# Kernel optimization log

Hardware: AMD Instinct MI355X
Metric: run time of the kernel (lower is better)

Reference implementation:

```python
import jax, jax.numpy as jnp
import numpy as np
from jax import lax

B, S = 256, 512
CHAR_NUM, CLASS_NUM, OUTPUT_NUM, WORD_EMBED, H = 10, 10, 64, 32, 128
EPS = 1e-12


def setup_inputs() -> dict:
    key = jax.random.key(0)
    ks = jax.random.split(key, 16)
    def nrm(k, shape, s=0.05):
        return jax.random.normal(k, shape, dtype=jnp.float32) * s
    return {
        "char_ids": jax.random.randint(ks[0], (B, S), 0, CHAR_NUM),
        "word_ids": jax.random.randint(ks[1], (B, S), 0, CHAR_NUM),
        "subject_ids": jax.random.randint(ks[2], (B, 2), 0, S),
        "emb_char": nrm(ks[3], (CHAR_NUM, OUTPUT_NUM)),
        "emb_word": nrm(ks[4], (CHAR_NUM, WORD_EMBED)),
        "Wwc": nrm(ks[5], (WORD_EMBED, OUTPUT_NUM)),
        "bwc": jnp.zeros((OUTPUT_NUM,), jnp.float32),
        "l1_Wx": nrm(ks[6], (OUTPUT_NUM, 4 * H)),
        "l1_Wh": nrm(ks[7], (H, 4 * H)),
        "l1_b": jnp.zeros((4 * H,), jnp.float32),
        "l2_Wx": nrm(ks[8], (H, 4 * H)),
        "l2_Wh": nrm(ks[9], (H, 4 * H)),
        "l2_b": jnp.zeros((4 * H,), jnp.float32),
        "beta_W": nrm(ks[10], (2 * H, H)),
        "beta_b": jnp.zeros((H,), jnp.float32),
        "gamma_W": nrm(ks[11], (2 * H, H)),
        "gamma_b": jnp.zeros((H,), jnp.float32),
        "sub_W": nrm(ks[12], (H, 2)),
        "sub_b": jnp.zeros((2,), jnp.float32),
        "po_W": nrm(ks[13], (H, 2 * CLASS_NUM)),
        "po_b": jnp.zeros((2 * CLASS_NUM,), jnp.float32),
    }


def _lstm_cell(x, h, c, Wx, Wh, b):
    # Keras LSTMCell: gates ordered i, f, g(cell), o
    z = x @ Wx + h @ Wh + b
    i, f, g, o = jnp.split(z, 4, axis=-1)
    c_new = jax.nn.sigmoid(f) * c + jax.nn.sigmoid(i) * jnp.tanh(g)
    h_new = jax.nn.sigmoid(o) * jnp.tanh(c_new)
    return h_new, c_new


def reference(char_ids, word_ids, subject_ids,
              emb_char, emb_word, Wwc, bwc,
              l1_Wx, l1_Wh, l1_b, l2_Wx, l2_Wh, l2_b,
              beta_W, beta_b, gamma_W, gamma_b,
              sub_W, sub_b, po_W, po_b):
    b, s = char_ids.shape
    # NOTE: source passes mask = (char_ids == 0) to the RNN; in Keras, mask True
    # means the step IS processed, so only positions with id==0 update state.
    step_mask = (char_ids == 0)  # [B, S] bool

    emb = emb_char[char_ids] + (emb_word[word_ids] @ Wwc + bwc)  # [B, S, 64]

    def step(carry, inp):
        h1, c1, h2, c2 = carry
        xt, mt = inp  # xt [B, 64], mt [B]
        h1n, c1n = _lstm_cell(xt, h1, c1, l1_Wx, l1_Wh, l1_b)
        h2n, c2n = _lstm_cell(h1n, h2, c2, l2_Wx, l2_Wh, l2_b)
        m = mt[:, None]
        h1 = jnp.where(m, h1n, h1)
        c1 = jnp.where(m, c1n, c1)
        h2 = jnp.where(m, h2n, h2)
        c2 = jnp.where(m, c2n, c2)
        return (h1, c1, h2, c2), h2

    z = jnp.zeros((b, H), emb.dtype)
    _, outs = lax.scan(step, (z, z, z, z),
                       (emb.transpose(1, 0, 2), step_mask.T))
    sent = outs.transpose(1, 0, 2)  # [B, S, 128]

    # vectorized batch_gather (replaces eager numpy per-row loop)
    bidx = jnp.arange(b)
    sub_start = sent[bidx, subject_ids[:, 0]]  # [B, 128]
    sub_end = sent[bidx, subject_ids[:, 1]]    # [B, 128]
    subject = jnp.concatenate([sub_start, sub_end], axis=1)  # [B, 256]

    # conditional layer norm
    beta = subject @ beta_W + beta_b    # [B, 128]
    gamma = subject @ gamma_W + gamma_b
    u = jnp.mean(sent, axis=-1, keepdims=True)
    v = jnp.mean((sent - u) ** 2, axis=-1, keepdims=True)
    xhat = (sent - u) / jnp.sqrt(v + EPS)
    context = gamma[:, None, :] * xhat + beta[:, None, :]  # [B, S, 128]

    # (transformer_encoder LSTM(32) output is dead code in the source; omitted)
    sub_preds = sent @ sub_W + sub_b                     # [B, S, 2]
    po_preds = (context @ po_W + po_b).reshape(b, -1, CLASS_NUM, 2)  # [B, S, 10, 2]
    return sub_preds, po_preds
```

## Files before the change

kernel.cpp:

```cpp
#include <hip/hip_runtime.h>
#include <cstdint>
#include <cstddef>


#define SLOTS 192

typedef _Float16 f16x2 __attribute__((ext_vector_type(2)));

__device__ __forceinline__ f16x2 as_h2(unsigned int v) {
    union { unsigned int u; f16x2 h; } x; x.u = v; return x.h;
}

#if __has_builtin(__builtin_amdgcn_fdot2)
__device__ __forceinline__ float fdot2(f16x2 a, f16x2 b, float c) {
    return __builtin_amdgcn_fdot2(a, b, c, false);
}
#else
__device__ __forceinline__ float fdot2(f16x2 a, f16x2 b, float c) {
    return c + (float)a.x * (float)b.x + (float)a.y * (float)b.y;
}
#endif

__device__ __forceinline__ float fast_rcp(float x) {
#if __has_builtin(__builtin_amdgcn_rcpf)
    return __builtin_amdgcn_rcpf(x);
#else
    return 1.f / x;
#endif
}
__device__ __forceinline__ float sigm(float x) {
    x = fminf(fmaxf(x, -30.f), 30.f);
    return fast_rcp(1.f + __expf(-x));
}
__device__ __forceinline__ float tanh_fast(float x) {
    x = fminf(fmaxf(x, -15.f), 15.f);
    float e = __expf(-2.f * x);
    return (1.f - e) * fast_rcp(1.f + e);
}

__device__ __forceinline__ float dpp_bfly4(float v) {
    union { float f; int i; } a, b;
    a.f = v;
    b.i = __builtin_amdgcn_update_dpp(0, a.i, 0xB1, 0xf, 0xf, true);
    a.f += b.f;
    b.i = __builtin_amdgcn_update_dpp(0, a.i, 0x4E, 0xf, 0xf, true);
    a.f += b.f;
    return a.f;
}

__device__ __forceinline__ float dot_u4(float s, const uint4 h, const uint4 w) {
    s = fdot2(as_h2(h.x), as_h2(w.x), s);
    s = fdot2(as_h2(h.y), as_h2(w.y), s);
    s = fdot2(as_h2(h.z), as_h2(w.z), s);
    s = fdot2(as_h2(h.w), as_h2(w.w), s);
    return s;
}

__global__ void k_xw1(const float* __restrict__ emb_char,
                      const float* __restrict__ emb_word,
                      const float* __restrict__ Wwc,
                      const float* __restrict__ bwc,
                      const float* __restrict__ l1_Wx,
                      const float* __restrict__ l1_b,
                      float* __restrict__ XW1) {
    __shared__ float xw[64];
    const int w = blockIdx.x;
    const int T = threadIdx.x;
    if (T < 64) {
        float acc = emb_char[T] + bwc[T];
        for (int m = 0; m < 32; ++m) acc += emb_word[w * 32 + m] * Wwc[m * 64 + T];
        xw[T] = acc;
    }
    __syncthreads();
    float acc = l1_b[T];
    for (int k = 0; k < 64; ++k) acc += xw[k] * l1_Wx[k * 512 + T];
    XW1[w * 512 + T] = acc;
}

__global__ void k_pack2(const float* __restrict__ l1_Wh,
                        const float* __restrict__ l2_Wx,
                        const float* __restrict__ l2_Wh,
                        uint4* __restrict__ W1H, uint4* __restrict__ W2H) {
    const int gid = blockIdx.x * blockDim.x + threadIdx.x;
    union { uint4 qv; f16x2 h[4]; } out;
    if (gid < 8192) {
        const int t = gid >> 4, i = gid & 15;
        const int q = t & 3, u = t >> 2;
        const int j = i >> 2, m = i & 3;
        const int col = u + 128 * j;
        for (int e = 0; e < 4; ++e) {
            const int k = 32 * q + 2 * (4 * m + e);
            f16x2 p;
            p.x = (_Float16)l1_Wh[k * 512 + col];
            p.y = (_Float16)l1_Wh[(k + 1) * 512 + col];
            out.h[e] = p;
        }
        W1H[gid] = out.qv;
    } else {
        const int gid2 = gid - 8192;
        const int t = gid2 >> 5, i = gid2 & 31;
        const int q = t & 3, u = t >> 2;
        const int ph = i >> 4, jm = i & 15;
        const int j = jm >> 2, m = jm & 3;
        const int col = u + 128 * j;
        const float* __restrict__ src = ph ? l2_Wx : l2_Wh;
        for (int e = 0; e < 4; ++e) {
            const int k = 32 * q + 2 * (4 * m + e);
            f16x2 p;
            p.x = (_Float16)src[k * 512 + col];
            p.y = (_Float16)src[(k + 1) * 512 + col];
            out.h[e] = p;
        }
        W2H[gid2] = out.qv;
    }
}

__global__ __launch_bounds__(512, 2) void k_lstm(
    const int* __restrict__ char_ids, const int* __restrict__ word_ids,
    const float* __restrict__ XW1, const uint4* __restrict__ W1H,
    const uint4* __restrict__ W2H, const float* __restrict__ l2_b,
    float* __restrict__ hbuf, unsigned short* __restrict__ idxbuf)
{
    const int b    = blockIdx.x;
    const int T    = threadIdx.x;
    const int lane = T & 63;
    const int wv   = T >> 6;
    const int q    = T & 3;
    const int u    = T >> 2;

    __shared__ int   charL[512];
    __shared__ int   wordL[512];
    __shared__ float XW1L[5120];
    __shared__ __align__(16) _Float16 h1f[2][128];
    __shared__ __align__(16) _Float16 h2f[128];
    __shared__ short actT[512];
    __shared__ int   ccnt[8];

    charL[T] = char_ids[b * 512 + T];
    wordL[T] = word_ids[b * 512 + T];
#pragma unroll
    for (int i = 0; i < 10; ++i) XW1L[i * 512 + T] = XW1[i * 512 + T];
    __syncthreads();

    const bool act = (charL[T] == 0);
    const unsigned long long bmask = __ballot(act);
    if (lane == 0) ccnt[wv] = (int)__popcll(bmask);
    __syncthreads();
    int base = 0;
    for (int i = 0; i < wv; ++i) base += ccnt[i];
    int tot = base;
    for (int i = wv; i < 8; ++i) tot += ccnt[i];
    if (act) actT[base + (int)__popcll(bmask & ((1ull << lane) - 1ull))] = (short)T;
    {
        int cin = base + (int)__popcll(bmask & ((2ull << lane) - 1ull));
        idxbuf[b * 512 + T] = (unsigned short)(cin < SLOTS - 1 ? cin : SLOTS - 1);
    }
    const int nact = tot;

    if (T < 128) {
        h1f[0][T] = (_Float16)0.f;
        h1f[1][T] = (_Float16)0.f;
        h2f[T]    = (_Float16)0.f;
        hbuf[(size_t)b * SLOTS * 128 + T] = 0.f;
    }
    float c1 = 0.f, c2 = 0.f;
    const float l2b0 = l2_b[u];
    const float l2b1 = l2_b[128 + u];
    const float l2b2 = l2_b[256 + u];
    const float l2b3 = l2_b[384 + u];

    uint4 w1[16], w2[32];
    {
        const uint4* W1t = W1H + (size_t)T * 16;
        const uint4* W2t = W2H + (size_t)T * 32;
#pragma unroll
        for (int i = 0; i < 16; ++i) w1[i] = W1t[i];
#pragma unroll
        for (int i = 0; i < 32; ++i) w2[i] = W2t[i];
    }
#pragma unroll
    for (int i = 0; i < 16; ++i)
        asm volatile("" : "+v"(w1[i].x), "+v"(w1[i].y), "+v"(w1[i].z), "+v"(w1[i].w));
#pragma unroll
    for (int i = 0; i < 32; ++i)
        asm volatile("" : "+v"(w2[i].x), "+v"(w2[i].y), "+v"(w2[i].z), "+v"(w2[i].w));

    __syncthreads();

    for (int a = 0; a < nact; ++a) {
        const int t   = actT[a];
        const int wid = wordL[t];
        const int cur = a & 1;

        const float xwi = XW1L[wid * 512 + u];
        const float xwf = XW1L[wid * 512 + 128 + u];
        const float xwg = XW1L[wid * 512 + 256 + u];
        const float xwo = XW1L[wid * 512 + 384 + u];

        const uint4* h1r = (const uint4*)&h1f[cur][0];
        const uint4 a0 = h1r[4 * q + 0];
        const uint4 a1 = h1r[4 * q + 1];
        const uint4 a2 = h1r[4 * q + 2];
        const uint4 a3 = h1r[4 * q + 3];
        const uint4* h2r = (const uint4*)h2f;
        const uint4 g0 = h2r[4 * q + 0];
        const uint4 g1 = h2r[4 * q + 1];
        const uint4 g2 = h2r[4 * q + 2];
        const uint4 g3 = h2r[4 * q + 3];

        float acc[4];
#pragma unroll
        for (int j = 0; j < 4; ++j) {
            float s = dot_u4(0.f, a0, w1[4 * j + 0]);
            s = dot_u4(s, a1, w1[4 * j + 1]);
            s = dot_u4(s, a2, w1[4 * j + 2]);
            s = dot_u4(s, a3, w1[4 * j + 3]);
            acc[j] = s;
        }

        const float zi = dpp_bfly4(acc[0]) + xwi;
        const float zf = dpp_bfly4(acc[1]) + xwf;
        const float zg = dpp_bfly4(acc[2]) + xwg;
        const float zo = dpp_bfly4(acc[3]) + xwo;
        c1 = sigm(zf) * c1 + sigm(zi) * tanh_fast(zg);
        const float h1n = sigm(zo) * tanh_fast(c1);
        if (q == 0) h1f[cur ^ 1][u] = (_Float16)h1n;

        float p[4];
#pragma unroll
        for (int j = 0; j < 4; ++j) {
            float s = dot_u4(0.f, g0, w2[4 * j + 0]);
            s = dot_u4(s, g1, w2[4 * j + 1]);
            s = dot_u4(s, g2, w2[4 * j + 2]);
            s = dot_u4(s, g3, w2[4 * j + 3]);
            p[j] = s;
        }
        __syncthreads();

        const uint4* h1nr = (const uint4*)&h1f[cur ^ 1][0];
        const uint4 e0 = h1nr[4 * q + 0];
        const uint4 e1 = h1nr[4 * q + 1];
        const uint4 e2 = h1nr[4 * q + 2];
        const uint4 e3 = h1nr[4 * q + 3];
#pragma unroll
        for (int j = 0; j < 4; ++j) {
            float s = p[j];
            s = dot_u4(s, e0, w2[16 + 4 * j + 0]);
            s = dot_u4(s, e1, w2[16 + 4 * j + 1]);
            s = dot_u4(s, e2, w2[16 + 4 * j + 2]);
            s = dot_u4(s, e3, w2[16 + 4 * j + 3]);
            p[j] = s;
        }
        const float y0 = dpp_bfly4(p[0]) + l2b0;
        const float y1 = dpp_bfly4(p[1]) + l2b1;
        const float y2 = dpp_bfly4(p[2]) + l2b2;
        const float y3 = dpp_bfly4(p[3]) + l2b3;
        c2 = sigm(y1) * c2 + sigm(y0) * tanh_fast(y2);
        const float h2v = sigm(y3) * tanh_fast(c2);
        if (q == 0) {
            h2f[u] = (_Float16)h2v;
            const int slot = (a + 1 < SLOTS - 1) ? a + 1 : SLOTS - 1;
            hbuf[((size_t)b * SLOTS + slot) * 128 + u] = h2v;
        }
        __syncthreads();
    }
}

__global__ void k_subject(const int* __restrict__ subject_ids,
                          const unsigned short* __restrict__ idxbuf,
                          const float* __restrict__ hbuf,
                          const float* __restrict__ beta_W, const float* __restrict__ beta_b,
                          const float* __restrict__ gamma_W, const float* __restrict__ gamma_b,
                          float* __restrict__ betaO, float* __restrict__ gammaO)
{
    const int b = blockIdx.x;
    const int u = threadIdx.x;
    __shared__ float subj[256];
    const int s0 = subject_ids[b * 2 + 0];
    const int s1 = subject_ids[b * 2 + 1];
    const int i0 = idxbuf[b * 512 + s0];
    const int i1 = idxbuf[b * 512 + s1];
    subj[u]       = hbuf[((size_t)b * SLOTS + i0) * 128 + u];
    subj[128 + u] = hbuf[((size_t)b * SLOTS + i1) * 128 + u];
    __syncthreads();
    float ab = beta_b[u], ag = gamma_b[u];
    for (int c = 0; c < 256; ++c) {
        const float s = subj[c];
        ab += s * beta_W[c * 128 + u];
        ag += s * gamma_W[c * 128 + u];
    }
    betaO[b * 128 + u]  = ab;
    gammaO[b * 128 + u] = ag;
}

__global__ __launch_bounds__(256) void k_out2(
    const unsigned short* __restrict__ idxbuf, const float* __restrict__ hbuf,
    const float* __restrict__ betaO, const float* __restrict__ gammaO,
    const float* __restrict__ sub_W, const float* __restrict__ sub_b,
    const float* __restrict__ po_W, const float* __restrict__ po_b,
    float* __restrict__ out)
{
    const int b = blockIdx.x;
    const int T = threadIdx.x;
    __shared__ float A[20][132];
    __shared__ float K1[20], K2[20];
    __shared__ float gm[128], bt[128];
    __shared__ float urs[192][2];
    __shared__ float povals[192 * 20];
    __shared__ float subv[192 * 2];
    __shared__ unsigned short idxr[512];
    __shared__ float swl[256];

    if (T < 128) { gm[T] = gammaO[b * 128 + T]; bt[T] = betaO[b * 128 + T]; }
    idxr[T] = idxbuf[b * 512 + T];
    idxr[256 + T] = idxbuf[b * 512 + 256 + T];
    swl[T] = sub_W[T];
    __syncthreads();

    for (int i = T; i < 2560; i += 256) {
        const int o = i >> 7, c = i & 127;
        A[o][c] = gm[c] * po_W[c * 20 + o];
    }
    if (T < 20) {
        float k1 = po_b[T], k2 = 0.f;
        for (int c = 0; c < 128; ++c) {
            const float pw = po_W[c * 20 + T];
            k1 += bt[c] * pw;
            k2 += gm[c] * pw;
        }
        K1[T] = k1; K2[T] = k2;
    }
    const int nslot = (int)idxr[511] + 1;
    const float sb0 = sub_b[0], sb1 = sub_b[1];
    for (int s = T; s < nslot; s += 256) {
        const float4* hp4 = (const float4*)(hbuf + ((size_t)b * SLOTS + s) * 128);
        float sum = 0.f, s2 = 0.f, sub0 = sb0, sub1 = sb1;
        for (int c4 = 0; c4 < 32; ++c4) {
            const float4 h = hp4[c4];
            sum += (h.x + h.y) + (h.z + h.w);
            s2  += h.x * h.x + h.y * h.y + h.z * h.z + h.w * h.w;
            const int c = 4 * c4;
            sub0 += h.x * swl[2 * c] + h.y * swl[2 * c + 2] + h.z * swl[2 * c + 4] + h.w * swl[2 * c + 6];
            sub1 += h.x * swl[2 * c + 1] + h.y * swl[2 * c + 3] + h.z * swl[2 * c + 5] + h.w * swl[2 * c + 7];
        }
        const float u = sum * (1.f / 128.f);
        const float v = fmaxf(s2 * (1.f / 128.f) - u * u, 0.f);
        urs[s][0] = u;
        urs[s][1] = 1.f / sqrtf(v + 1e-12f);
        subv[2 * s] = sub0; subv[2 * s + 1] = sub1;
    }
    __syncthreads();

    for (int i = T; i < nslot * 20; i += 256) {
        const int s = i / 20, o = i - 20 * s;
        const float u = urs[s][0], rs = urs[s][1];
        const float4* hp4 = (const float4*)(hbuf + ((size_t)b * SLOTS + s) * 128);
        const float* Ao = &A[o][0];
        float acc = 0.f;
        for (int c4 = 0; c4 < 32; ++c4) {
            const float4 h = hp4[c4];
            const float4 aa = *(const float4*)&Ao[4 * c4];
            acc += h.x * aa.x + h.y * aa.y + h.z * aa.z + h.w * aa.w;
        }
        povals[i] = rs * acc - u * rs * K2[o] + K1[o];
    }
    __syncthreads();

    for (int i = T; i < 2560; i += 256) {
        const int t = i / 5, j = i - 5 * t;
        const int sl = idxr[t];
        const float4 v = *(const float4*)&povals[sl * 20 + 4 * j];
        *(float4*)&out[262144 + ((size_t)(b * 512 + t)) * 20 + 4 * j] = v;
    }
    for (int i = T; i < 512; i += 256) {
        const int sl = idxr[i];
        float2 v; v.x = subv[2 * sl]; v.y = subv[2 * sl + 1];
        *(float2*)&out[((size_t)(b * 512 + i)) * 2] = v;
    }
}

extern "C" void kernel_launch(void* const* d_in, const int* in_sizes, int n_in,
                              void* d_out, int out_size, void* d_ws, size_t ws_size,
                              hipStream_t stream) {
    (void)in_sizes; (void)n_in; (void)out_size; (void)ws_size;
    const int*   char_ids    = (const int*)d_in[0];
    const int*   word_ids    = (const int*)d_in[1];
    const int*   subject_ids = (const int*)d_in[2];
    const float* emb_char    = (const float*)d_in[3];
    const float* emb_word    = (const float*)d_in[4];
    const float* Wwc         = (const float*)d_in[5];
    const float* bwc         = (const float*)d_in[6];
    const float* l1_Wx       = (const float*)d_in[7];
    const float* l1_Wh       = (const float*)d_in[8];
    const float* l1_b        = (const float*)d_in[9];
    const float* l2_Wx       = (const float*)d_in[10];
    const float* l2_Wh       = (const float*)d_in[11];
    const float* l2_b        = (const float*)d_in[12];
    const float* beta_W      = (const float*)d_in[13];
    const float* beta_b      = (const float*)d_in[14];
    const float* gamma_W     = (const float*)d_in[15];
    const float* gamma_b     = (const float*)d_in[16];
    const float* sub_W       = (const float*)d_in[17];
    const float* sub_b       = (const float*)d_in[18];
    const float* po_W        = (const float*)d_in[19];
    const float* po_b        = (const float*)d_in[20];
    float* out = (float*)d_out;

    char* ws = (char*)d_ws;
    float*          XW1    = (float*)(ws + 0);
    uint4*          W1H    = (uint4*)(ws + 32768);
    uint4*          W2H    = (uint4*)(ws + 163840);
    float*          betaO  = (float*)(ws + 425984);
    float*          gammaO = (float*)(ws + 557056);
    unsigned short* idxbuf = (unsigned short*)(ws + 688128);
    float*          hbuf   = (float*)(ws + 950272);

    k_xw1<<<dim3(10), dim3(512), 0, stream>>>(emb_char, emb_word, Wwc, bwc, l1_Wx, l1_b, XW1);
    k_pack2<<<dim3(96), dim3(256), 0, stream>>>(l1_Wh, l2_Wx, l2_Wh, W1H, W2H);
    k_lstm<<<dim3(256), dim3(512), 0, stream>>>(char_ids, word_ids, XW1, W1H, W2H,
                                                l2_b, hbuf, idxbuf);
    k_subject<<<dim3(256), dim3(128), 0, stream>>>(subject_ids, idxbuf, hbuf,
                                                   beta_W, beta_b, gamma_W, gamma_b,
                                                   betaO, gammaO);
    k_out2<<<dim3(256), dim3(256), 0, stream>>>(idxbuf, hbuf, betaO, gammaO,
                                                sub_W, sub_b, po_W, po_b, out);
}
```

Baseline: 246.0 us.

## Skew LSTM layers to one barrier per step and split subject GEMV

The two-layer recurrence is skewed: layer 1 for step a+1 is computed in the same phase as layer 2 for step a, since both read the same h1 value. Double-buffering h2 lets each step need a single __syncthreads instead of two, which shortens the serial critical path of the recurrence. A prologue computes the first layer-1 step, and the loop is manually unrolled by two to alternate buffers. Separately, k_subject now uses 256 threads so beta and gamma are computed by different halves of the block, halving the serial loop per thread.

```diff
diff --git a/kernel.cpp b/kernel.cpp
--- a/kernel.cpp
+++ b/kernel.cpp
@@ -132,7 +132,7 @@
     __shared__ int   wordL[512];
     __shared__ float XW1L[5120];
     __shared__ __align__(16) _Float16 h1f[2][128];
-    __shared__ __align__(16) _Float16 h2f[128];
+    __shared__ __align__(16) _Float16 h2f[2][128];
     __shared__ short actT[512];
     __shared__ int   ccnt[8];
 
@@ -160,7 +160,8 @@
     if (T < 128) {
         h1f[0][T] = (_Float16)0.f;
         h1f[1][T] = (_Float16)0.f;
-        h2f[T]    = (_Float16)0.f;
+        h2f[0][T] = (_Float16)0.f;
+        h2f[1][T] = (_Float16)0.f;
         hbuf[(size_t)b * SLOTS * 128 + T] = 0.f;
     }
     float c1 = 0.f, c2 = 0.f;
@@ -187,110 +188,123 @@
 
     __syncthreads();
 
-    for (int a = 0; a < nact; ++a) {
-        const int t   = actT[a];
-        const int wid = wordL[t];
-        const int cur = a & 1;
-
-        const float xwi = XW1L[wid * 512 + u];
-        const float xwf = XW1L[wid * 512 + 128 + u];
-        const float xwg = XW1L[wid * 512 + 256 + u];
-        const float xwo = XW1L[wid * 512 + 384 + u];
-
-        const uint4* h1r = (const uint4*)&h1f[cur][0];
-        const uint4 a0 = h1r[4 * q + 0];
-        const uint4 a1 = h1r[4 * q + 1];
-        const uint4 a2 = h1r[4 * q + 2];
-        const uint4 a3 = h1r[4 * q + 3];
-        const uint4* h2r = (const uint4*)h2f;
-        const uint4 g0 = h2r[4 * q + 0];
-        const uint4 g1 = h2r[4 * q + 1];
-        const uint4 g2 = h2r[4 * q + 2];
-        const uint4 g3 = h2r[4 * q + 3];
-
-        float acc[4];
-#pragma unroll
-        for (int j = 0; j < 4; ++j) {
-            float s = dot_u4(0.f, a0, w1[4 * j + 0]);
-            s = dot_u4(s, a1, w1[4 * j + 1]);
-            s = dot_u4(s, a2, w1[4 * j + 2]);
-            s = dot_u4(s, a3, w1[4 * j + 3]);
-            acc[j] = s;
-        }
-
-        const float zi = dpp_bfly4(acc[0]) + xwi;
-        const float zf = dpp_bfly4(acc[1]) + xwf;
-        const float zg = dpp_bfly4(acc[2]) + xwg;
-        const float zo = dpp_bfly4(acc[3]) + xwo;
-        c1 = sigm(zf) * c1 + sigm(zi) * tanh_fast(zg);
+    if (nact > 0) {
+        const int w0_ = wordL[actT[0]];
+        const float zi = XW1L[w0_ * 512 + u];
+        const float zg = XW1L[w0_ * 512 + 256 + u];
+        const float zo = XW1L[w0_ * 512 + 384 + u];
+        c1 = sigm(zi) * tanh_fast(zg);
         const float h1n = sigm(zo) * tanh_fast(c1);
-        if (q == 0) h1f[cur ^ 1][u] = (_Float16)h1n;
-
-        float p[4];
-#pragma unroll
-        for (int j = 0; j < 4; ++j) {
-            float s = dot_u4(0.f, g0, w2[4 * j + 0]);
-            s = dot_u4(s, g1, w2[4 * j + 1]);
-            s = dot_u4(s, g2, w2[4 * j + 2]);
-            s = dot_u4(s, g3, w2[4 * j + 3]);
-            p[j] = s;
-        }
+        if (q == 0) h1f[0][u] = (_Float16)h1n;
         __syncthreads();
-
-        const uint4* h1nr = (const uint4*)&h1f[cur ^ 1][0];
-        const uint4 e0 = h1nr[4 * q + 0];
-        const uint4 e1 = h1nr[4 * q + 1];
-        const uint4 e2 = h1nr[4 * q + 2];
-        const uint4 e3 = h1nr[4 * q + 3];
-#pragma unroll
-        for (int j = 0; j < 4; ++j) {
-            float s = p[j];
-            s = dot_u4(s, e0, w2[16 + 4 * j + 0]);
-            s = dot_u4(s, e1, w2[16 + 4 * j + 1]);
-            s = dot_u4(s, e2, w2[16 + 4 * j + 2]);
-            s = dot_u4(s, e3, w2[16 + 4 * j + 3]);
-            p[j] = s;
-        }
-        const float y0 = dpp_bfly4(p[0]) + l2b0;
-        const float y1 = dpp_bfly4(p[1]) + l2b1;
-        const float y2 = dpp_bfly4(p[2]) + l2b2;
-        const float y3 = dpp_bfly4(p[3]) + l2b3;
-        c2 = sigm(y1) * c2 + sigm(y0) * tanh_fast(y2);
-        const float h2v = sigm(y3) * tanh_fast(c2);
-        if (q == 0) {
-            h2f[u] = (_Float16)h2v;
-            const int slot = (a + 1 < SLOTS - 1) ? a + 1 : SLOTS - 1;
-            hbuf[((size_t)b * SLOTS + slot) * 128 + u] = h2v;
-        }
-        __syncthreads();
-    }
-}
-
-__global__ void k_subject(const int* __restrict__ subject_ids,
-                          const unsigned short* __restrict__ idxbuf,
-                          const float* __restrict__ hbuf,
-                          const float* __restrict__ beta_W, const float* __restrict__ beta_b,
-                          const float* __restrict__ gamma_W, const float* __restrict__ gamma_b,
-                          float* __restrict__ betaO, float* __restrict__ gammaO)
+    }
+
+#define LSTM_STEP(H1S, H2S, H1D, H2D)                                          \
+    {                                                                          \
+        const uint4* h1r = (const uint4*)&H1S[0] + 4 * q;                      \
+        const uint4 a0 = h1r[0], a1 = h1r[1], a2 = h1r[2], a3 = h1r[3];        \
+        const uint4* h2r = (const uint4*)&H2S[0] + 4 * q;                      \
+        const uint4 g0 = h2r[0], g1 = h2r[1], g2 = h2r[2], g3 = h2r[3];        \
+        const bool more = (a + 1 < nact);                                      \
+        const int wid = more ? wordL[actT[a + 1]] : 0;                         \
+        const float xwi = XW1L[wid * 512 + u];                                 \
+        const float xwf = XW1L[wid * 512 + 128 + u];                           \
+        const float xwg = XW1L[wid * 512 + 256 + u];                           \
+        const float xwo = XW1L[wid * 512 + 384 + u];                           \
+        float p[4];                                                            \
+        _Pragma("unroll")                                                      \
+        for (int j = 0; j < 4; ++j) {                                          \
+            float s = dot_u4(0.f, g0, w2[4 * j + 0]);                          \
+            s = dot_u4(s, g1, w2[4 * j + 1]);                                  \
+            s = dot_u4(s, g2, w2[4 * j + 2]);                                  \
+            s = dot_u4(s, g3, w2[4 * j + 3]);                                  \
+            s = dot_u4(s, a0, w2[16 + 4 * j + 0]);                             \
+            s = dot_u4(s, a1, w2[16 + 4 * j + 1]);                             \
+            s = dot_u4(s, a2, w2[16 + 4 * j + 2]);                             \
+            s = dot_u4(s, a3, w2[16 + 4 * j + 3]);                             \
+            p[j] = s;                                                          \
+        }                                                                      \
+        const float y0 = dpp_bfly4(p[0]) + l2b0;                               \
+        const float y1 = dpp_bfly4(p[1]) + l2b1;                               \
+        const float y2 = dpp_bfly4(p[2]) + l2b2;                               \
+        const float y3 = dpp_bfly4(p[3]) + l2b3;                               \
+        c2 = sigm(y1) * c2 + sigm(y0) * tanh_fast(y2);                         \
+        const float h2v = sigm(y3) * tanh_fast(c2);                            \
+        if (q == 0) {                                                          \
+            H2D[u] = (_Float16)h2v;                                            \
+            const int slot = (a + 1 < SLOTS - 1) ? a + 1 : SLOTS - 1;          \
+            hbuf[((size_t)b * SLOTS + slot) * 128 + u] = h2v;                  \
+        }                                                                      \
+        if (more) {                                                            \
+            float r0, r1, r2, r3;                                              \
+            {                                                                  \
+                float r = dot_u4(0.f, a0, w1[0]);                              \
+                r = dot_u4(r, a1, w1[1]);                                      \
+                r = dot_u4(r, a2, w1[2]);                                      \
+                r = dot_u4(r, a3, w1[3]);                                      \
+                r0 = r;                                                        \
+                r = dot_u4(0.f, a0, w1[4]);                                    \
+                r = dot_u4(r, a1, w1[5]);                                      \
+                r = dot_u4(r, a2, w1[6]);                                      \
+                r = dot_u4(r, a3, w1[7]);                                      \
+                r1 = r;                                                        \
+                r = dot_u4(0.f, a0, w1[8]);                                    \
+                r = dot_u4(r, a1, w1[9]);                                      \
+                r = dot_u4(r, a2, w1[10]);                                     \
+                r = dot_u4(r, a3, w1[11]);                                     \
+                r2 = r;                                                        \
+                r = dot_u4(0.f, a0, w1[12]);                                   \
+                r = dot_u4(r, a1, w1[13]);                                     \
+                r = dot_u4(r, a2, w1[14]);                                     \
+                r = dot_u4(r, a3, w1[15]);                                     \
+                r3 = r;                                                        \
+            }                                                                  \
+            const float zi = dpp_bfly4(r0) + xwi;                              \
+            const float zf = dpp_bfly4(r1) + xwf;                              \
+            const float zg = dpp_bfly4(r2) + xwg;                              \
+            const float zo = dpp_bfly4(r3) + xwo;                              \
+            c1 = sigm(zf) * c1 + sigm(zi) * tanh_fast(zg);                     \
+            const float h1n = sigm(zo) * tanh_fast(c1);                        \
+            if (q == 0) H1D[u] = (_Float16)h1n;                                \
+        }                                                                      \
+        __syncthreads();                                                       \
+    }
+
+    int a = 0;
+    while (a < nact) {
+        LSTM_STEP(h1f[0], h2f[0], h1f[1], h2f[1]);
+        ++a;
+        if (a >= nact) break;
+        LSTM_STEP(h1f[1], h2f[1], h1f[0], h2f[0]);
+        ++a;
+    }
+#undef LSTM_STEP
+}
+
+__global__ __launch_bounds__(256) void k_subject(
+    const int* __restrict__ subject_ids,
+    const unsigned short* __restrict__ idxbuf,
+    const float* __restrict__ hbuf,
+    const float* __restrict__ beta_W, const float* __restrict__ beta_b,
+    const float* __restrict__ gamma_W, const float* __restrict__ gamma_b,
+    float* __restrict__ betaO, float* __restrict__ gammaO)
 {
     const int b = blockIdx.x;
-    const int u = threadIdx.x;
+    const int T = threadIdx.x;
+    const int u = T & 127, half = T >> 7;
     __shared__ float subj[256];
     const int s0 = subject_ids[b * 2 + 0];
     const int s1 = subject_ids[b * 2 + 1];
     const int i0 = idxbuf[b * 512 + s0];
     const int i1 = idxbuf[b * 512 + s1];
-    subj[u]       = hbuf[((size_t)b * SLOTS + i0) * 128 + u];
-    subj[128 + u] = hbuf[((size_t)b * SLOTS + i1) * 128 + u];
-    __syncthreads();
-    float ab = beta_b[u], ag = gamma_b[u];
-    for (int c = 0; c < 256; ++c) {
-        const float s = subj[c];
-        ab += s * beta_W[c * 128 + u];
-        ag += s * gamma_W[c * 128 + u];
-    }
-    betaO[b * 128 + u]  = ab;
-    gammaO[b * 128 + u] = ag;
+    const int slot = half ? i1 : i0;
+    subj[T] = hbuf[((size_t)b * SLOTS + slot) * 128 + u];
+    __syncthreads();
+    const float* __restrict__ W = half ? gamma_W : beta_W;
+    float acc = half ? gamma_b[u] : beta_b[u];
+    for (int c = 0; c < 256; ++c) acc += subj[c] * W[c * 128 + u];
+    if (half) gammaO[b * 128 + u] = acc;
+    else      betaO[b * 128 + u]  = acc;
 }
 
 __global__ __launch_bounds__(256) void k_out2(
@@ -419,7 +433,7 @@
     k_pack2<<<dim3(96), dim3(256), 0, stream>>>(l1_Wh, l2_Wx, l2_Wh, W1H, W2H);
     k_lstm<<<dim3(256), dim3(512), 0, stream>>>(char_ids, word_ids, XW1, W1H, W2H,
                                                 l2_b, hbuf, idxbuf);
-    k_subject<<<dim3(256), dim3(128), 0, stream>>>(subject_ids, idxbuf, hbuf,
+    k_subject<<<dim3(256), dim3(256), 0, stream>>>(subject_ids, idxbuf, hbuf,
                                                    beta_W, beta_b, gamma_W, gamma_b,
                                                    betaO, gammaO);
     k_out2<<<dim3(256), dim3(256), 0, stream>>>(idxbuf, hbuf, betaO, gammaO,
```

New measurement: 244.7 us. No clear change (-0.5%).
